# Kernel optimization log

Hardware: AMD Instinct MI355X
Metric: run time of the kernel (lower is better)

## Reference

```python
import jax, jax.numpy as jnp
import numpy as np

B, S, D, H = 2, 2048, 1024, 16
DK = D // H

def setup_inputs() -> dict:
    key = jax.random.key(0)
    ks = jax.random.split(key, 9)
    s = 1.0 / np.sqrt(D)
    return {
        "query": jax.random.normal(ks[0], (B, S, D), dtype=jnp.float32),
        "Wq": jax.random.uniform(ks[1], (D, D), jnp.float32, -s, s),
        "bq": jax.random.uniform(ks[2], (D,), jnp.float32, -s, s),
        "Wk": jax.random.uniform(ks[3], (D, D), jnp.float32, -s, s),
        "bk": jax.random.uniform(ks[4], (D,), jnp.float32, -s, s),
        "Wv": jax.random.uniform(ks[5], (D, D), jnp.float32, -s, s),
        "bv": jax.random.uniform(ks[6], (D,), jnp.float32, -s, s),
        "Wo": jax.random.uniform(ks[7], (D, D), jnp.float32, -s, s),
        "bo": jax.random.uniform(ks[8], (D,), jnp.float32, -s, s),
    }

def reference(query, Wq, bq, Wk, bk, Wv, bv, Wo, bo):
    # q/k/v projections, reshape to [B,H,S,DK]
    def proj(x, W, b):
        return (x @ W + b).reshape(B, S, H, DK).transpose(0, 2, 1, 3)
    q = proj(query, Wq, bq)
    k = proj(query, Wk, bk)
    v = proj(query, Wv, bv)
    scores = jnp.einsum("bhqd,bhkd->bhqk", q, k) / jnp.sqrt(jnp.float32(DK))
    attn = jax.nn.softmax(scores, axis=-1)
    out = jnp.einsum("bhqk,bhkd->bhqd", attn, v)  # [B,H,S,DK]
    concat = out.transpose(0, 2, 1, 3).reshape(B, S, D)
    return concat @ Wo + bo
```

## Files before the change

kernel.cpp:

```cpp
#include <hip/hip_runtime.h>

#define S_LEN  2048
#define DMODEL 1024
#define NHEAD  16
#define DKDIM  64
#define NBATCH 2

typedef short bf16x8 __attribute__((ext_vector_type(8)));
typedef float f32x4  __attribute__((ext_vector_type(4)));

__device__ __forceinline__ unsigned short f2b(float f){
  unsigned int x = __float_as_uint(f);
  return (unsigned short)((x + 0x7FFFu + ((x >> 16) & 1u)) >> 16);
}
__device__ __forceinline__ unsigned short f2b_rhu(float f){
  return (unsigned short)((__float_as_uint(f) + 0x8000u) >> 16);
}
__device__ __forceinline__ bf16x8 ld8(const unsigned short* p){
  return *reinterpret_cast<const bf16x8*>(p);
}
__device__ __forceinline__ void gld16(const unsigned short* g, unsigned short* l){
  __builtin_amdgcn_global_load_lds(
      (const __attribute__((address_space(1))) unsigned int*)(uintptr_t)g,
      (__attribute__((address_space(3))) unsigned int*)(uintptr_t)l,
      16, 0, 0);
}

__global__ __launch_bounds__(256) void convert_x(
    const float* __restrict__ X, unsigned short* __restrict__ Xc)
{
  const size_t i0 = ((size_t)blockIdx.x * 256 + threadIdx.x) * 8;
  const float4 a = *reinterpret_cast<const float4*>(X + i0);
  const float4 b = *reinterpret_cast<const float4*>(X + i0 + 4);
  bf16x8 o;
  o[0]=(short)f2b(a.x); o[1]=(short)f2b(a.y); o[2]=(short)f2b(a.z); o[3]=(short)f2b(a.w);
  o[4]=(short)f2b(b.x); o[5]=(short)f2b(b.y); o[6]=(short)f2b(b.z); o[7]=(short)f2b(b.w);
  *reinterpret_cast<bf16x8*>(Xc + i0) = o;
}

__global__ __launch_bounds__(256) void transpose_w(
    const float* __restrict__ W0, const float* __restrict__ W1,
    const float* __restrict__ W2, const float* __restrict__ W3,
    unsigned short* __restrict__ Wt)
{
  __shared__ unsigned short tile[64][65];
  const float* src = (blockIdx.z==0)?W0:(blockIdx.z==1)?W1:(blockIdx.z==2)?W2:W3;
  unsigned short* dst = Wt + (size_t)blockIdx.z * DMODEL * DMODEL;
  const int r0 = blockIdx.x * 64, c0 = blockIdx.y * 64;
  #pragma unroll
  for(int t=0;t<16;t++){
    int idx = threadIdx.x + t*256;
    int r = idx >> 6, c = idx & 63;
    tile[r][c] = f2b(src[(size_t)(r0+r)*DMODEL + (c0+c)]);
  }
  __syncthreads();
  #pragma unroll
  for(int t=0;t<16;t++){
    int idx = threadIdx.x + t*256;
    int r = idx >> 6, c = idx & 63;
    dst[(size_t)(c0+r)*DMODEL + (r0+c)] = tile[c][r];
  }
}

__global__ __launch_bounds__(256) void gemm_qkv(
    const unsigned short* __restrict__ Xc,
    const unsigned short* __restrict__ WtBase,
    const float* __restrict__ bq,
    const float* __restrict__ bk,
    const float* __restrict__ bv,
    unsigned short* __restrict__ q_ws,
    unsigned short* __restrict__ k_ws,
    unsigned short* __restrict__ vT_ws)
{
  __shared__ __align__(16) unsigned short sA[128][32];
  __shared__ __align__(16) unsigned short sB[128][32];
  __shared__ __align__(16) unsigned short sT[64*136];
  const int z = blockIdx.z;
  const unsigned short* Wt   = WtBase + (size_t)z * DMODEL * DMODEL;
  const float* bias = (z==0) ? bq : ((z==1) ? bk : bv);
  const int m0 = blockIdx.x * 128, n0 = blockIdx.y * 128;
  const int tid = threadIdx.x;
  const int w = tid >> 6, lane = tid & 63, quad = lane >> 4, lm = lane & 15;
  const int wm = (w & 1) * 64, wn = (w >> 1) * 64;
  const int srow = lane >> 2, scol = (lane & 3) * 8;

  f32x4 acc[4][4];
  #pragma unroll
  for(int i=0;i<4;i++)
    #pragma unroll
    for(int j=0;j<4;j++){ f32x4 z4 = {0.f,0.f,0.f,0.f}; acc[i][j] = z4; }

  for(int k0=0;k0<DMODEL;k0+=32){
    #pragma unroll
    for(int j=0;j<2;j++){
      gld16(Xc + (size_t)(m0 + w*32 + j*16 + srow)*DMODEL + k0 + scol, &sA[w*32 + j*16][0]);
      gld16(Wt + (size_t)(n0 + w*32 + j*16 + srow)*DMODEL + k0 + scol, &sB[w*32 + j*16][0]);
    }
    __syncthreads();
    bf16x8 a[4], b[4];
    #pragma unroll
    for(int i=0;i<4;i++) a[i] = ld8(&sA[wm + i*16 + lm][quad*8]);
    #pragma unroll
    for(int j=0;j<4;j++) b[j] = ld8(&sB[wn + j*16 + lm][quad*8]);
    #pragma unroll
    for(int i=0;i<4;i++)
      #pragma unroll
      for(int j=0;j<4;j++)
        acc[i][j] = __builtin_amdgcn_mfma_f32_16x16x32_bf16(a[i], b[j], acc[i][j], 0, 0, 0);
    __syncthreads();
  }

  if(z != 2){
    #pragma unroll
    for(int j=0;j<4;j++){
      const int n  = n0 + wn + j*16 + lm;
      const float bb = bias[n];
      const int h_ = n >> 6, d_ = n & 63;
      #pragma unroll
      for(int i=0;i<4;i++){
        #pragma unroll
        for(int r=0;r<4;r++){
          const int m  = m0 + wm + i*16 + quad*4 + r;
          const int b_ = m >> 11, s_ = m & 2047;
          const unsigned short o = f2b(acc[i][j][r] + bb);
          if(z == 0) q_ws[((size_t)(b_*NHEAD + h_)*S_LEN + s_)*DKDIM + d_] = o;
          else       k_ws[((size_t)(b_*NHEAD + h_)*S_LEN + s_)*DKDIM + d_] = o;
        }
      }
    }
  } else {
    #pragma unroll
    for(int hf=0; hf<2; hf++){
      if((w >> 1) == hf){
        #pragma unroll
        for(int j=0;j<4;j++){
          const int nl = j*16 + lm;
          const float bb = bias[n0 + hf*64 + nl];
          #pragma unroll
          for(int i=0;i<4;i++)
            #pragma unroll
            for(int r=0;r<4;r++)
              sT[nl*136 + wm + i*16 + quad*4 + r] = f2b(acc[i][j][r] + bb);
        }
      }
      __syncthreads();
      {
        const int nl = tid >> 2, seg = tid & 3;
        const int n  = n0 + hf*64 + nl;
        const int h_ = n >> 6, d_ = n & 63;
        const int b_ = m0 >> 11;
        const int s0 = (m0 & 2047) + seg*32;
        unsigned short* dst = vT_ws + ((size_t)(b_*NHEAD + h_)*DKDIM + d_)*S_LEN + s0;
        #pragma unroll
        for(int k=0;k<4;k++)
          *reinterpret_cast<bf16x8*>(dst + k*8) =
              *reinterpret_cast<const bf16x8*>(&sT[nl*136 + seg*32 + k*8]);
      }
      __syncthreads();
    }
  }
}

__global__ __launch_bounds__(256) void flash_attn(
    const unsigned short* __restrict__ q_ws,
    const unsigned short* __restrict__ k_ws,
    const unsigned short* __restrict__ vT_ws,
    unsigned short* __restrict__ attn_c)
{
  __shared__ __align__(16) unsigned short kt[2][64][72];
  __shared__ __align__(16) unsigned short vt[2][64][72];
  __shared__ __align__(16) unsigned short ph[4][16][40];
  const int bh = blockIdx.y;
  const int b_ = bh >> 4, h_ = bh & 15;
  const int tid = threadIdx.x;
  const int w = tid >> 6, lane = tid & 63, quad = lane >> 4, lm = lane & 15;
  const int r0 = blockIdx.x * 64 + w * 16;

  const unsigned short* qp = q_ws  + ((size_t)bh * S_LEN + r0) * DKDIM;
  const unsigned short* kp = k_ws  + (size_t)bh * S_LEN * DKDIM;
  const unsigned short* vp = vT_ws + (size_t)bh * DKDIM * S_LEN;

  bf16x8 qf0 = ld8(qp + (size_t)lm*DKDIM + quad*8);
  bf16x8 qf1 = ld8(qp + (size_t)lm*DKDIM + 32 + quad*8);

  f32x4 o_acc[4];
  #pragma unroll
  for(int d=0;d<4;d++){ f32x4 z4 = {0.f,0.f,0.f,0.f}; o_acc[d] = z4; }
  float rsum[4] = {0.f,0.f,0.f,0.f};

  const int srow = lane >> 3;
  const int scol = (lane & 7) * 8;

  bf16x8 kreg[2], vreg[2];
  #pragma unroll
  for(int p=0;p<2;p++){
    kreg[p] = ld8(kp + (size_t)(w*16 + p*8 + srow)*DKDIM + scol);
    vreg[p] = ld8(vp + (size_t)(w*16 + p*8 + srow)*S_LEN + scol);
  }
  #pragma unroll
  for(int p=0;p<2;p++){
    *reinterpret_cast<bf16x8*>(&kt[0][w*16 + p*8 + srow][scol]) = kreg[p];
    *reinterpret_cast<bf16x8*>(&vt[0][w*16 + p*8 + srow][scol]) = vreg[p];
  }
  __syncthreads();

  for(int t=0;t<32;t++){
    const int buf = t & 1;
    if(t < 31){
      const int jn = (t+1)*64;
      #pragma unroll
      for(int p=0;p<2;p++){
        kreg[p] = ld8(kp + (size_t)(jn + w*16 + p*8 + srow)*DKDIM + scol);
        vreg[p] = ld8(vp + (size_t)(w*16 + p*8 + srow)*S_LEN + jn + scol);
      }
    }
    #pragma unroll
    for(int sh=0;sh<2;sh++){
      #pragma unroll
      for(int s2=0;s2<2;s2++){
        const int s = sh*2 + s2;
        bf16x8 k0 = ld8(&kt[buf][s*16 + lm][quad*8]);
        bf16x8 k1 = ld8(&kt[buf][s*16 + lm][32 + quad*8]);
        f32x4 z4 = {0.f,0.f,0.f,0.f};
        f32x4 sc = __builtin_amdgcn_mfma_f32_16x16x32_bf16(qf0, k0, z4, 0,0,0);
        sc       = __builtin_amdgcn_mfma_f32_16x16x32_bf16(qf1, k1, sc, 0,0,0);
        #pragma unroll
        for(int r=0;r<4;r++){
          float e = __expf(sc[r]*0.125f);
          rsum[r] += e;
          ph[w][quad*4 + r][s2*16 + lm] = f2b_rhu(e);
        }
      }
      bf16x8 pf = ld8(&ph[w][lm][quad*8]);
      #pragma unroll
      for(int d=0;d<4;d++){
        bf16x8 vf = ld8(&vt[buf][d*16 + lm][sh*32 + quad*8]);
        o_acc[d] = __builtin_amdgcn_mfma_f32_16x16x32_bf16(pf, vf, o_acc[d], 0,0,0);
      }
    }
    if(t < 31){
      const int nb = 1 - buf;
      #pragma unroll
      for(int p=0;p<2;p++){
        *reinterpret_cast<bf16x8*>(&kt[nb][w*16 + p*8 + srow][scol]) = kreg[p];
        *reinterpret_cast<bf16x8*>(&vt[nb][w*16 + p*8 + srow][scol]) = vreg[p];
      }
    }
    __syncthreads();
  }

  float rinv[4];
  #pragma unroll
  for(int r=0;r<4;r++){
    float s = rsum[r];
    s += __shfl_xor(s,1);
    s += __shfl_xor(s,2);
    s += __shfl_xor(s,4);
    s += __shfl_xor(s,8);
    rinv[r] = __frcp_rn(s);
  }

  #pragma unroll
  for(int d=0;d<4;d++)
    #pragma unroll
    for(int r=0;r<4;r++){
      const int row = r0 + quad*4 + r;
      const int col = h_*DKDIM + d*16 + lm;
      attn_c[((size_t)(b_*S_LEN + row))*DMODEL + col] = f2b(o_acc[d][r] * rinv[r]);
    }
}

__global__ __launch_bounds__(256) void gemm_out(
    const unsigned short* __restrict__ A,
    const unsigned short* __restrict__ Wt,
    const float* __restrict__ bias,
    float* __restrict__ out)
{
  __shared__ __align__(16) unsigned short sA[128][32];
  __shared__ __align__(16) unsigned short sB[128][32];
  const int m0 = blockIdx.x * 128, n0 = blockIdx.y * 128;
  const int tid = threadIdx.x;
  const int w = tid >> 6, lane = tid & 63, quad = lane >> 4, lm = lane & 15;
  const int wm = (w & 1) * 64, wn = (w >> 1) * 64;
  const int srow = lane >> 2, scol = (lane & 3) * 8;

  f32x4 acc[4][4];
  #pragma unroll
  for(int i=0;i<4;i++)
    #pragma unroll
    for(int j=0;j<4;j++){ f32x4 z4 = {0.f,0.f,0.f,0.f}; acc[i][j] = z4; }

  for(int k0=0;k0<DMODEL;k0+=32){
    #pragma unroll
    for(int j=0;j<2;j++){
      gld16(A  + (size_t)(m0 + w*32 + j*16 + srow)*DMODEL + k0 + scol, &sA[w*32 + j*16][0]);
      gld16(Wt + (size_t)(n0 + w*32 + j*16 + srow)*DMODEL + k0 + scol, &sB[w*32 + j*16][0]);
    }
    __syncthreads();
    bf16x8 a[4], b[4];
    #pragma unroll
    for(int i=0;i<4;i++) a[i] = ld8(&sA[wm + i*16 + lm][quad*8]);
    #pragma unroll
    for(int j=0;j<4;j++) b[j] = ld8(&sB[wn + j*16 + lm][quad*8]);
    #pragma unroll
    for(int i=0;i<4;i++)
      #pragma unroll
      for(int j=0;j<4;j++)
        acc[i][j] = __builtin_amdgcn_mfma_f32_16x16x32_bf16(a[i], b[j], acc[i][j], 0, 0, 0);
    __syncthreads();
  }

  #pragma unroll
  for(int j=0;j<4;j++){
    const int n = n0 + wn + j*16 + lm;
    const float bb = bias[n];
    #pragma unroll
    for(int i=0;i<4;i++){
      #pragma unroll
      for(int r=0;r<4;r++){
        const int m = m0 + wm + i*16 + quad*4 + r;
        out[(size_t)m*DMODEL + n] = acc[i][j][r] + bb;
      }
    }
  }
}

extern "C" void kernel_launch(void* const* d_in, const int* in_sizes, int n_in,
                              void* d_out, int out_size, void* d_ws, size_t ws_size,
                              hipStream_t stream)
{
  const float* X  = (const float*)d_in[0];
  const float* Wq = (const float*)d_in[1];
  const float* bq = (const float*)d_in[2];
  const float* Wk = (const float*)d_in[3];
  const float* bk = (const float*)d_in[4];
  const float* Wv = (const float*)d_in[5];
  const float* bv = (const float*)d_in[6];
  const float* Wo = (const float*)d_in[7];
  const float* bo = (const float*)d_in[8];

  unsigned short* ws = (unsigned short*)d_ws;
  const size_t WMAT = (size_t)DMODEL * DMODEL;
  const size_t QKV  = (size_t)NBATCH * NHEAD * S_LEN * DKDIM;
  unsigned short* Wt     = ws;
  unsigned short* Xc     = ws + 4*WMAT;
  unsigned short* q_ws   = Xc + QKV;
  unsigned short* k_ws   = q_ws + QKV;
  unsigned short* vT_ws  = k_ws + QKV;
  unsigned short* attn_c = Xc;
  float* out = (float*)d_out;

  convert_x  <<<dim3(2048),     256, 0, stream>>>(X, Xc);
  transpose_w<<<dim3(16,16,4),  256, 0, stream>>>(Wq, Wk, Wv, Wo, Wt);
  gemm_qkv   <<<dim3(32,8,3),   256, 0, stream>>>(Xc, Wt, bq, bk, bv, q_ws, k_ws, vT_ws);
  flash_attn <<<dim3(32,32),    256, 0, stream>>>(q_ws, k_ws, vT_ws, attn_c);
  gemm_out   <<<dim3(32,8),     256, 0, stream>>>(attn_c, Wt + 3*WMAT, bo, out);
}
```

Before: 228.2 us.

## Fold softmax scale into Wq, deepen GEMM K-step, simplify V store and attention buffers

Result: slower. 236.7 us (+3.7%).

```diff
diff --git a/kernel.cpp b/kernel.cpp
--- a/kernel.cpp
+++ b/kernel.cpp
@@ -45,13 +45,14 @@
 {
   __shared__ unsigned short tile[64][65];
   const float* src = (blockIdx.z==0)?W0:(blockIdx.z==1)?W1:(blockIdx.z==2)?W2:W3;
+  const float sc = (blockIdx.z==0) ? 0.125f : 1.0f;
   unsigned short* dst = Wt + (size_t)blockIdx.z * DMODEL * DMODEL;
   const int r0 = blockIdx.x * 64, c0 = blockIdx.y * 64;
   #pragma unroll
   for(int t=0;t<16;t++){
     int idx = threadIdx.x + t*256;
     int r = idx >> 6, c = idx & 63;
-    tile[r][c] = f2b(src[(size_t)(r0+r)*DMODEL + (c0+c)]);
+    tile[r][c] = f2b(src[(size_t)(r0+r)*DMODEL + (c0+c)] * sc);
   }
   __syncthreads();
   #pragma unroll
@@ -72,12 +73,12 @@
     unsigned short* __restrict__ k_ws,
     unsigned short* __restrict__ vT_ws)
 {
-  __shared__ __align__(16) unsigned short sA[128][32];
-  __shared__ __align__(16) unsigned short sB[128][32];
-  __shared__ __align__(16) unsigned short sT[64*136];
+  __shared__ __align__(16) unsigned short sA[2][128][32];
+  __shared__ __align__(16) unsigned short sB[2][128][32];
   const int z = blockIdx.z;
   const unsigned short* Wt   = WtBase + (size_t)z * DMODEL * DMODEL;
   const float* bias = (z==0) ? bq : ((z==1) ? bk : bv);
+  const float bscale = (z==0) ? 0.125f : 1.0f;
   const int m0 = blockIdx.x * 128, n0 = blockIdx.y * 128;
   const int tid = threadIdx.x;
   const int w = tid >> 6, lane = tid & 63, quad = lane >> 4, lm = lane & 15;
@@ -90,73 +91,47 @@
     #pragma unroll
     for(int j=0;j<4;j++){ f32x4 z4 = {0.f,0.f,0.f,0.f}; acc[i][j] = z4; }
 
-  for(int k0=0;k0<DMODEL;k0+=32){
-    #pragma unroll
-    for(int j=0;j<2;j++){
-      gld16(Xc + (size_t)(m0 + w*32 + j*16 + srow)*DMODEL + k0 + scol, &sA[w*32 + j*16][0]);
-      gld16(Wt + (size_t)(n0 + w*32 + j*16 + srow)*DMODEL + k0 + scol, &sB[w*32 + j*16][0]);
-    }
-    __syncthreads();
-    bf16x8 a[4], b[4];
-    #pragma unroll
-    for(int i=0;i<4;i++) a[i] = ld8(&sA[wm + i*16 + lm][quad*8]);
-    #pragma unroll
-    for(int j=0;j<4;j++) b[j] = ld8(&sB[wn + j*16 + lm][quad*8]);
-    #pragma unroll
-    for(int i=0;i<4;i++)
-      #pragma unroll
-      for(int j=0;j<4;j++)
-        acc[i][j] = __builtin_amdgcn_mfma_f32_16x16x32_bf16(a[i], b[j], acc[i][j], 0, 0, 0);
-    __syncthreads();
-  }
-
-  if(z != 2){
-    #pragma unroll
-    for(int j=0;j<4;j++){
-      const int n  = n0 + wn + j*16 + lm;
-      const float bb = bias[n];
-      const int h_ = n >> 6, d_ = n & 63;
-      #pragma unroll
-      for(int i=0;i<4;i++){
+  for(int k0=0;k0<DMODEL;k0+=64){
+    #pragma unroll
+    for(int c=0;c<2;c++)
+      #pragma unroll
+      for(int j=0;j<2;j++){
+        gld16(Xc + (size_t)(m0 + w*32 + j*16 + srow)*DMODEL + k0 + c*32 + scol, &sA[c][w*32 + j*16][0]);
+        gld16(Wt + (size_t)(n0 + w*32 + j*16 + srow)*DMODEL + k0 + c*32 + scol, &sB[c][w*32 + j*16][0]);
+      }
+    __syncthreads();
+    #pragma unroll
+    for(int c=0;c<2;c++){
+      bf16x8 a[4], b[4];
+      #pragma unroll
+      for(int i=0;i<4;i++) a[i] = ld8(&sA[c][wm + i*16 + lm][quad*8]);
+      #pragma unroll
+      for(int j=0;j<4;j++) b[j] = ld8(&sB[c][wn + j*16 + lm][quad*8]);
+      #pragma unroll
+      for(int i=0;i<4;i++)
         #pragma unroll
-        for(int r=0;r<4;r++){
-          const int m  = m0 + wm + i*16 + quad*4 + r;
-          const int b_ = m >> 11, s_ = m & 2047;
-          const unsigned short o = f2b(acc[i][j][r] + bb);
-          if(z == 0) q_ws[((size_t)(b_*NHEAD + h_)*S_LEN + s_)*DKDIM + d_] = o;
-          else       k_ws[((size_t)(b_*NHEAD + h_)*S_LEN + s_)*DKDIM + d_] = o;
-        }
-      }
-    }
-  } else {
-    #pragma unroll
-    for(int hf=0; hf<2; hf++){
-      if((w >> 1) == hf){
-        #pragma unroll
-        for(int j=0;j<4;j++){
-          const int nl = j*16 + lm;
-          const float bb = bias[n0 + hf*64 + nl];
-          #pragma unroll
-          for(int i=0;i<4;i++)
-            #pragma unroll
-            for(int r=0;r<4;r++)
-              sT[nl*136 + wm + i*16 + quad*4 + r] = f2b(acc[i][j][r] + bb);
-        }
-      }
-      __syncthreads();
-      {
-        const int nl = tid >> 2, seg = tid & 3;
-        const int n  = n0 + hf*64 + nl;
-        const int h_ = n >> 6, d_ = n & 63;
-        const int b_ = m0 >> 11;
-        const int s0 = (m0 & 2047) + seg*32;
-        unsigned short* dst = vT_ws + ((size_t)(b_*NHEAD + h_)*DKDIM + d_)*S_LEN + s0;
-        #pragma unroll
-        for(int k=0;k<4;k++)
-          *reinterpret_cast<bf16x8*>(dst + k*8) =
-              *reinterpret_cast<const bf16x8*>(&sT[nl*136 + seg*32 + k*8]);
-      }
-      __syncthreads();
+        for(int j=0;j<4;j++)
+          acc[i][j] = __builtin_amdgcn_mfma_f32_16x16x32_bf16(a[i], b[j], acc[i][j], 0, 0, 0);
+    }
+    __syncthreads();
+  }
+
+  #pragma unroll
+  for(int j=0;j<4;j++){
+    const int n  = n0 + wn + j*16 + lm;
+    const float bb = bias[n] * bscale;
+    const int h_ = n >> 6, d_ = n & 63;
+    #pragma unroll
+    for(int i=0;i<4;i++){
+      #pragma unroll
+      for(int r=0;r<4;r++){
+        const int m  = m0 + wm + i*16 + quad*4 + r;
+        const int b_ = m >> 11, s_ = m & 2047;
+        const unsigned short o = f2b(acc[i][j][r] + bb);
+        if(z == 0)      q_ws [((size_t)(b_*NHEAD + h_)*S_LEN + s_)*DKDIM + d_] = o;
+        else if(z == 1) k_ws [((size_t)(b_*NHEAD + h_)*S_LEN + s_)*DKDIM + d_] = o;
+        else            vT_ws[((size_t)(b_*NHEAD + h_)*DKDIM + d_)*S_LEN + s_] = o;
+      }
     }
   }
 }
@@ -167,8 +142,8 @@
     const unsigned short* __restrict__ vT_ws,
     unsigned short* __restrict__ attn_c)
 {
-  __shared__ __align__(16) unsigned short kt[2][64][72];
-  __shared__ __align__(16) unsigned short vt[2][64][72];
+  __shared__ __align__(16) unsigned short kt[64][72];
+  __shared__ __align__(16) unsigned short vt[64][72];
   __shared__ __align__(16) unsigned short ph[4][16][40];
   const int bh = blockIdx.y;
   const int b_ = bh >> 4, h_ = bh & 15;
@@ -199,13 +174,12 @@
   }
   #pragma unroll
   for(int p=0;p<2;p++){
-    *reinterpret_cast<bf16x8*>(&kt[0][w*16 + p*8 + srow][scol]) = kreg[p];
-    *reinterpret_cast<bf16x8*>(&vt[0][w*16 + p*8 + srow][scol]) = vreg[p];
+    *reinterpret_cast<bf16x8*>(&kt[w*16 + p*8 + srow][scol]) = kreg[p];
+    *reinterpret_cast<bf16x8*>(&vt[w*16 + p*8 + srow][scol]) = vreg[p];
   }
   __syncthreads();
 
   for(int t=0;t<32;t++){
-    const int buf = t & 1;
     if(t < 31){
       const int jn = (t+1)*64;
       #pragma unroll
@@ -219,14 +193,14 @@
       #pragma unroll
       for(int s2=0;s2<2;s2++){
         const int s = sh*2 + s2;
-        bf16x8 k0 = ld8(&kt[buf][s*16 + lm][quad*8]);
-        bf16x8 k1 = ld8(&kt[buf][s*16 + lm][32 + quad*8]);
+        bf16x8 k0 = ld8(&kt[s*16 + lm][quad*8]);
+        bf16x8 k1 = ld8(&kt[s*16 + lm][32 + quad*8]);
         f32x4 z4 = {0.f,0.f,0.f,0.f};
         f32x4 sc = __builtin_amdgcn_mfma_f32_16x16x32_bf16(qf0, k0, z4, 0,0,0);
         sc       = __builtin_amdgcn_mfma_f32_16x16x32_bf16(qf1, k1, sc, 0,0,0);
         #pragma unroll
         for(int r=0;r<4;r++){
-          float e = __expf(sc[r]*0.125f);
+          float e = __expf(sc[r]);
           rsum[r] += e;
           ph[w][quad*4 + r][s2*16 + lm] = f2b_rhu(e);
         }
@@ -234,16 +208,16 @@
       bf16x8 pf = ld8(&ph[w][lm][quad*8]);
       #pragma unroll
       for(int d=0;d<4;d++){
-        bf16x8 vf = ld8(&vt[buf][d*16 + lm][sh*32 + quad*8]);
+        bf16x8 vf = ld8(&vt[d*16 + lm][sh*32 + quad*8]);
         o_acc[d] = __builtin_amdgcn_mfma_f32_16x16x32_bf16(pf, vf, o_acc[d], 0,0,0);
       }
     }
+    __syncthreads();
     if(t < 31){
-      const int nb = 1 - buf;
       #pragma unroll
       for(int p=0;p<2;p++){
-        *reinterpret_cast<bf16x8*>(&kt[nb][w*16 + p*8 + srow][scol]) = kreg[p];
-        *reinterpret_cast<bf16x8*>(&vt[nb][w*16 + p*8 + srow][scol]) = vreg[p];
+        *reinterpret_cast<bf16x8*>(&kt[w*16 + p*8 + srow][scol]) = kreg[p];
+        *reinterpret_cast<bf16x8*>(&vt[w*16 + p*8 + srow][scol]) = vreg[p];
       }
     }
     __syncthreads();
@@ -276,8 +250,8 @@
     const float* __restrict__ bias,
     float* __restrict__ out)
 {
-  __shared__ __align__(16) unsigned short sA[128][32];
-  __shared__ __align__(16) unsigned short sB[128][32];
+  __shared__ __align__(16) unsigned short sA[2][128][32];
+  __shared__ __align__(16) unsigned short sB[2][128][32];
   const int m0 = blockIdx.x * 128, n0 = blockIdx.y * 128;
   const int tid = threadIdx.x;
   const int w = tid >> 6, lane = tid & 63, quad = lane >> 4, lm = lane & 15;
@@ -290,23 +264,28 @@
     #pragma unroll
     for(int j=0;j<4;j++){ f32x4 z4 = {0.f,0.f,0.f,0.f}; acc[i][j] = z4; }
 
-  for(int k0=0;k0<DMODEL;k0+=32){
-    #pragma unroll
-    for(int j=0;j<2;j++){
-      gld16(A  + (size_t)(m0 + w*32 + j*16 + srow)*DMODEL + k0 + scol, &sA[w*32 + j*16][0]);
-      gld16(Wt + (size_t)(n0 + w*32 + j*16 + srow)*DMODEL + k0 + scol, &sB[w*32 + j*16][0]);
-    }
-    __syncthreads();
-    bf16x8 a[4], b[4];
-    #pragma unroll
-    for(int i=0;i<4;i++) a[i] = ld8(&sA[wm + i*16 + lm][quad*8]);
-    #pragma unroll
-    for(int j=0;j<4;j++) b[j] = ld8(&sB[wn + j*16 + lm][quad*8]);
-    #pragma unroll
-    for(int i=0;i<4;i++)
-      #pragma unroll
-      for(int j=0;j<4;j++)
-        acc[i][j] = __builtin_amdgcn_mfma_f32_16x16x32_bf16(a[i], b[j], acc[i][j], 0, 0, 0);
+  for(int k0=0;k0<DMODEL;k0+=64){
+    #pragma unroll
+    for(int c=0;c<2;c++)
+      #pragma unroll
+      for(int j=0;j<2;j++){
+        gld16(A  + (size_t)(m0 + w*32 + j*16 + srow)*DMODEL + k0 + c*32 + scol, &sA[c][w*32 + j*16][0]);
+        gld16(Wt + (size_t)(n0 + w*32 + j*16 + srow)*DMODEL + k0 + c*32 + scol, &sB[c][w*32 + j*16][0]);
+      }
+    __syncthreads();
+    #pragma unroll
+    for(int c=0;c<2;c++){
+      bf16x8 a[4], b[4];
+      #pragma unroll
+      for(int i=0;i<4;i++) a[i] = ld8(&sA[c][wm + i*16 + lm][quad*8]);
+      #pragma unroll
+      for(int j=0;j<4;j++) b[j] = ld8(&sB[c][wn + j*16 + lm][quad*8]);
+      #pragma unroll
+      for(int i=0;i<4;i++)
+        #pragma unroll
+        for(int j=0;j<4;j++)
+          acc[i][j] = __builtin_amdgcn_mfma_f32_16x16x32_bf16(a[i], b[j], acc[i][j], 0, 0, 0);
+    }
     __syncthreads();
   }
 
```
